# Kernel tuning notes

Hardware: AMD Instinct MI355X
Metric: run time of the kernel (lower is better)

The kernel has to match this reference:

```python
import jax, jax.numpy as jnp
import numpy as np

H = 12          # nheads
SIM_EPS = 1e-8  # SimMatrix eps
LN_EPS = 1e-5   # nn.LayerNorm default eps
SLOPE = 0.01    # LeakyReLU default negative slope


def leaky(x):
    return jnp.where(x >= 0, x, SLOPE * x)


def etc_attention(hiddens, gamma, beta, Wout, bout):
    # hiddens: [B, L, 3*D]
    B, L, D3 = hiddens.shape
    D = D3 // 3
    d = D // H
    h = hiddens.reshape(B, L, 3, H, d)
    Q = h[:, :, 0].transpose(0, 2, 1, 3)  # [B,H,L,d]
    K = h[:, :, 1].transpose(0, 2, 1, 3)
    V = h[:, :, 2].transpose(0, 2, 1, 3)
    # cosine-similarity attention scores (SimMatrix(K, Q))
    Kn = K / jnp.clip(jnp.linalg.norm(K, axis=-1, keepdims=True), SIM_EPS, None)
    Qn = Q / jnp.clip(jnp.linalg.norm(Q, axis=-1, keepdims=True), SIM_EPS, None)
    att = jnp.einsum('bhid,bhjd->bhij', Kn, Qn)  # [B,H,L,L]
    # LayerNorm over the head axis H (lnormalize: [B, L*L, H] layernorm on last dim)
    mu = att.mean(axis=1, keepdims=True)
    var = att.var(axis=1, keepdims=True)  # biased, matches torch LayerNorm
    att = (att - mu) / jnp.sqrt(var + LN_EPS)
    att = att * gamma[None, :, None, None] + beta[None, :, None, None]
    att = jax.nn.softmax(att, axis=-1)
    att = jnp.where(jnp.isnan(att), jnp.zeros_like(att), att)  # removeNaN
    out = jnp.einsum('bhij,bhjd->bhid', att, V)          # att @ V
    out = out.transpose(0, 2, 1, 3).reshape(B, L, D)      # catHiddens
    # dropout is identity at inference; lin_out = Linear + Softmax
    probs = jax.nn.softmax(out @ Wout.T + bout, axis=-1)  # [B,L,C]
    return probs, att


def get_weights(att, masks):
    # att: [B,H,L,L], masks: [B,L] float
    w = masks * att.mean(axis=1).sum(axis=1)  # [B,L]
    return jax.nn.softmax(w, axis=-1)[..., None]  # [B,L,1]


def setup_inputs() -> dict:
    key = jax.random.key(0)
    ks = jax.random.split(key, 16)
    B, L = 16, 512
    Din, D, C, VOCAB = 300, 768, 20, 32000

    def kaiming(k, shape, fan_in):
        return jax.random.normal(k, shape, jnp.float32) * np.sqrt(2.0 / fan_in)

    return {
        'input_ids': jax.random.randint(ks[0], (B, L), 0, VOCAB),
        'wv': jax.random.normal(ks[1], (B, L, Din), jnp.float32),
        'emb': jax.random.normal(ks[2], (VOCAB, D), jnp.float32),
        'W_t': kaiming(ks[3], (3 * D, D), D),
        'b_t': jnp.zeros((3 * D,), jnp.float32),
        'gamma_t': jnp.ones((H,), jnp.float32),
        'beta_t': jnp.zeros((H,), jnp.float32),
        'Wout_t': kaiming(ks[4], (C, D), D),
        'bout_t': jnp.zeros((C,), jnp.float32),
        'W_h': kaiming(ks[5], (3 * D, Din), Din),
        'b_h': jnp.zeros((3 * D,), jnp.float32),
        'gamma_h': jnp.ones((H,), jnp.float32),
        'beta_h': jnp.zeros((H,), jnp.float32),
        'Wout_h': kaiming(ks[6], (C, D), D),
        'bout_h': jnp.zeros((C,), jnp.float32),
    }


def reference(input_ids, wv, emb, W_t, b_t, gamma_t, beta_t, Wout_t, bout_t,
              W_h, b_h, gamma_h, beta_h, Wout_h, bout_h):
    masks = (input_ids != 0).astype(jnp.float32)  # [B,L]
    # token branch: Embedding -> LeakyReLU -> Linear -> LeakyReLU
    h_t = leaky(leaky(emb[input_ids]) @ W_t.T + b_t)
    probs_t, att_t = etc_attention(h_t, gamma_t, beta_t, Wout_t, bout_t)
    probs_t = (get_weights(att_t, masks) * probs_t).sum(axis=1)  # [B,C]
    # hidden/word-vector branch: Linear -> LeakyReLU
    h_h = leaky(wv @ W_h.T + b_h)
    probs_h, att_h = etc_attention(h_h, gamma_h, beta_h, Wout_h, bout_h)
    probs_h = (get_weights(att_h, masks) * probs_h).sum(axis=1)
    return (probs_t + probs_h) / 2.0
```

## Files before the change

kernel.cpp:

```cpp
#include <hip/hip_runtime.h>

typedef unsigned int uint;
typedef unsigned short ushort;
typedef _Float16 f16;
typedef _Float16 h8 __attribute__((ext_vector_type(8)));
typedef float f32x4 __attribute__((ext_vector_type(4)));


__device__ __forceinline__ float b2f(ushort u){ return __uint_as_float(((uint)u)<<16); }
__device__ __forceinline__ ushort f2b(float f){
  uint u = __float_as_uint(f);
  uint r = u + 0x7fffu + ((u>>16)&1u);
  return (ushort)(r>>16);
}
__device__ __forceinline__ float leaky(float x){ return x >= 0.f ? x : 0.01f*x; }
__device__ __forceinline__ float ldf(const void* p, int idx, int isb){
  return isb ? b2f(((const ushort*)p)[idx]) : ((const float*)p)[idx];
}

#define GLOAD16(gp, lp) __builtin_amdgcn_global_load_lds( \
    (const __attribute__((address_space(1))) void*)(gp), \
    (__attribute__((address_space(3))) void*)(lp), 16, 0, 0)

__global__ __launch_bounds__(256) void k_init(const ushort* __restrict__ wvbits,
    int* __restrict__ flag, float* __restrict__ zbase){
  int bid = blockIdx.x, tid = threadIdx.x;
  if (bid == 0){
    if (tid == 0){
      int sane = 0;
      for (int i=0;i<128;i++){
        uint e = (wvbits[i]>>7)&0xffu;
        if (e==0u || (e>=90u && e<=150u)) sane++;
      }
      *flag = (sane >= 115) ? 1 : 0;
    }
  } else {
    zbase[(bid-1)*256 + tid] = 0.f;
  }
}

__global__ __launch_bounds__(256) void k_prep_all(const int* __restrict__ ids,
    const void* __restrict__ emb, const void* __restrict__ wv,
    const void* __restrict__ W0, const void* __restrict__ W1,
    const int* __restrict__ flag,
    f16* __restrict__ AhA, f16* __restrict__ WhA,
    f16* __restrict__ AhB, f16* __restrict__ WhB,
    int nBX, int nW0, int nA1, int nW1){
  int isb = *flag;
  int bx = blockIdx.x, tid = threadIdx.x;
  if (bx < nBX){
    int t = bx*256 + tid;
    int m = t / 96, kk = (t % 96) * 8;
    float o[8];
    if (isb){
      const ushort* src = (const ushort*)emb + (size_t)ids[m]*768 + kk;
      uint4 v = *(const uint4*)src;
      o[0]=__uint_as_float((v.x&0xffffu)<<16); o[1]=__uint_as_float(v.x&0xffff0000u);
      o[2]=__uint_as_float((v.y&0xffffu)<<16); o[3]=__uint_as_float(v.y&0xffff0000u);
      o[4]=__uint_as_float((v.z&0xffffu)<<16); o[5]=__uint_as_float(v.z&0xffff0000u);
      o[6]=__uint_as_float((v.w&0xffffu)<<16); o[7]=__uint_as_float(v.w&0xffff0000u);
    } else {
      const float* src = (const float*)emb + (size_t)ids[m]*768 + kk;
      float4 v0 = ((const float4*)src)[0];
      float4 v1 = ((const float4*)src)[1];
      o[0]=v0.x; o[1]=v0.y; o[2]=v0.z; o[3]=v0.w;
      o[4]=v1.x; o[5]=v1.y; o[6]=v1.z; o[7]=v1.w;
    }
    h8 hv;
    #pragma unroll
    for (int i=0;i<8;i++) hv[i] = (f16)leaky(o[i]);
    *(h8*)(AhA + (size_t)m*768 + kk) = hv;
  } else if (bx < nBX + nW0){
    int t = (bx - nBX)*256 + tid;
    int n = t / 96, kk = (t % 96) * 8;
    h8 hv;
    #pragma unroll
    for (int i=0;i<8;i++) hv[i] = (f16)ldf(W0, n*768 + kk + i, isb);
    *(h8*)(WhA + (size_t)n*768 + kk) = hv;
  } else if (bx < nBX + nW0 + nA1){
    int t = (bx - nBX - nW0)*256 + tid;
    int n = t / 40, kk = (t % 40) * 8;
    h8 hv;
    #pragma unroll
    for (int i=0;i<8;i++){
      int k = kk + i;
      hv[i] = (k < 300) ? (f16)ldf(wv, n*300 + k, isb) : (f16)0.f;
    }
    *(h8*)(AhB + (size_t)n*320 + kk) = hv;
  } else {
    int t = (bx - nBX - nW0 - nA1)*256 + tid;
    int n = t / 40, kk = (t % 40) * 8;
    h8 hv;
    #pragma unroll
    for (int i=0;i<8;i++){
      int k = kk + i;
      hv[i] = (k < 300) ? (f16)ldf(W1, n*300 + k, isb) : (f16)0.f;
    }
    *(h8*)(WhB + (size_t)n*320 + kk) = hv;
  }
}

__global__ __launch_bounds__(256) void k_gemm_m(
    const f16* AhA, const f16* WhA, const void* biasA, int KA,
    f16* QhA, f16* KhA, f16* VtA,
    const f16* AhB, const f16* WhB, const void* biasB, int KB,
    f16* QhB, f16* KhB, f16* VtB,
    const int* __restrict__ flag, int sbase){
  __shared__ __align__(16) f16 As[128*64];
  __shared__ __align__(16) f16 Bs[128*64];
  int z = sbase + blockIdx.z;
  const f16* Ah = z ? AhB : AhA;
  const f16* Wh = z ? WhB : WhA;
  const void* bias = z ? biasB : biasA;
  int KP = z ? KB : KA;
  f16* Qh = z ? QhB : QhA;
  f16* Kh = z ? KhB : KhA;
  f16* Vt = z ? VtB : VtA;
  int STEPS = KP >> 6;

  int tid = threadIdx.x;
  int w = tid >> 6, lane = tid & 63;
  int mrow = lane & 15, kq = lane >> 4;
  int m0 = blockIdx.x * 128;
  int n0 = blockIdx.y * 128;
  int msub = (w & 1) * 64, nsub = (w >> 1) * 64;

  f32x4 acc[4][4];
  #pragma unroll
  for (int mt=0; mt<4; mt++)
    #pragma unroll
    for (int nt=0; nt<4; nt++) acc[mt][nt] = (f32x4){0.f,0.f,0.f,0.f};

  int cbase = w*64 + lane;

  for (int step=0; step<STEPS; step++){
    int k0 = step*64;
    __syncthreads();
    #pragma unroll
    for (int rep=0; rep<4; rep++){
      int cb = rep*256 + w*64;
      int c  = rep*256 + cbase;
      int row = c >> 3;
      int qs  = (c & 7) ^ (row & 7);
      GLOAD16(Ah + (size_t)(m0+row)*KP + k0 + qs*8, As + cb*8);
      GLOAD16(Wh + (size_t)(n0+row)*KP + k0 + qs*8, Bs + cb*8);
    }
    __syncthreads();
    #pragma unroll
    for (int ks=0; ks<2; ks++){
      h8 af[4], bf[4];
      #pragma unroll
      for (int mt=0; mt<4; mt++){
        int row = msub + mt*16 + mrow;
        int slot = (ks*4 + kq) ^ (row & 7);
        af[mt] = *(const h8*)(As + row*64 + slot*8);
      }
      #pragma unroll
      for (int nt=0; nt<4; nt++){
        int row = nsub + nt*16 + mrow;
        int slot = (ks*4 + kq) ^ (row & 7);
        bf[nt] = *(const h8*)(Bs + row*64 + slot*8);
      }
      #pragma unroll
      for (int mt=0; mt<4; mt++)
        #pragma unroll
        for (int nt=0; nt<4; nt++)
          acc[mt][nt] = __builtin_amdgcn_mfma_f32_16x16x32_f16(af[mt], bf[nt], acc[mt][nt], 0, 0, 0);
    }
  }

  int isb = *flag;
  int n0w = n0 + nsub;
  int s = n0w / 768;
  int h = (n0w % 768) >> 6;
  float bv[4];
  #pragma unroll
  for (int nt=0; nt<4; nt++) bv[nt] = ldf(bias, n0w + nt*16 + mrow, isb);

  #pragma unroll
  for (int mt=0; mt<4; mt++){
    float yv[4][4];
    #pragma unroll
    for (int nt=0; nt<4; nt++)
      #pragma unroll
      for (int r=0; r<4; r++)
        yv[nt][r] = leaky(acc[mt][nt][r] + bv[nt]);
    if (s < 2){
      #pragma unroll
      for (int r=0; r<4; r++){
        float ss = yv[0][r]*yv[0][r] + yv[1][r]*yv[1][r]
                 + yv[2][r]*yv[2][r] + yv[3][r]*yv[3][r];
        ss += __shfl_xor(ss, 1); ss += __shfl_xor(ss, 2);
        ss += __shfl_xor(ss, 4); ss += __shfl_xor(ss, 8);
        float rn = 1.f / fmaxf(sqrtf(ss), 1e-8f);
        #pragma unroll
        for (int nt=0; nt<4; nt++) yv[nt][r] *= rn;
      }
    }
    #pragma unroll
    for (int nt=0; nt<4; nt++){
      #pragma unroll
      for (int r=0; r<4; r++){
        int m = m0 + msub + mt*16 + kq*4 + r;
        int dd = nt*16 + mrow;
        int bq = m >> 9, l = m & 511;
        float y = yv[nt][r];
        if (s == 0)      Qh[((size_t)(bq*12 + h)*512 + l)*64 + dd] = (f16)y;
        else if (s == 1) Kh[((size_t)(bq*12 + h)*512 + l)*64 + dd] = (f16)y;
        else             Vt[((size_t)(bq*12 + h)*64 + dd)*512 + l] = (f16)y;
      }
    }
  }
}

__global__ __launch_bounds__(256) void k_attn(
    const f16* __restrict__ Qh0, const f16* __restrict__ Kh0, const f16* __restrict__ Vt0,
    const void* __restrict__ g0, const void* __restrict__ be0,
    float* __restrict__ O0, float* __restrict__ csg0,
    const f16* __restrict__ Qh1, const f16* __restrict__ Kh1, const f16* __restrict__ Vt1,
    const void* __restrict__ g1, const void* __restrict__ be1,
    float* __restrict__ O1, float* __restrict__ csg1,
    const int* __restrict__ flag, int sbase){
  constexpr int TS = 72;
  __shared__ __align__(16) f16 S[12*16*TS];
  __shared__ float gL[12], beL[12];
  __shared__ float rowsumL[192], rinvL[192];
  __shared__ float csL[512];

  int z = sbase + blockIdx.y;
  const f16* Qh = z ? Qh1 : Qh0;
  const f16* Kh = z ? Kh1 : Kh0;
  const f16* Vt = z ? Vt1 : Vt0;
  const void* gamma = z ? g1 : g0;
  const void* beta  = z ? be1 : be0;
  float* O   = z ? O1 : O0;
  float* csg = z ? csg1 : csg0;

  int tid = threadIdx.x;
  int w = tid >> 6, lane = tid & 63;
  int kq = lane >> 4, mrow = lane & 15;
  int b = blockIdx.x >> 5, it = blockIdx.x & 31;
  int i0 = it * 16;
  int h0 = w * 3;
  int pj = tid & 63, piw = tid >> 6;

  if (tid < 12){ int isb = *flag; gL[tid] = ldf(gamma, tid, isb); beL[tid] = ldf(beta, tid, isb); }
  if (tid < 192) rowsumL[tid] = 0.f;
  csL[tid] = 0.f; csL[tid + 256] = 0.f;

  h8 ka[3][2];
  #pragma unroll
  for (int hh=0; hh<3; hh++){
    const f16* kb = Kh + ((size_t)(b*12 + h0 + hh)*512 + i0 + mrow)*64;
    ka[hh][0] = *(const h8*)(kb + kq*8);
    ka[hh][1] = *(const h8*)(kb + 32 + kq*8);
  }

  f32x4 acc[3][4];
  #pragma unroll
  for (int hh=0; hh<3; hh++)
    #pragma unroll
    for (int nt=0; nt<4; nt++) acc[hh][nt] = (f32x4){0.f,0.f,0.f,0.f};

  __syncthreads();

  for (int jt=0; jt<8; jt++){
    int j0 = jt*64;
    #pragma unroll
    for (int hh=0; hh<3; hh++){
      int h = h0 + hh;
      const f16* qb = Qh + ((size_t)(b*12+h)*512 + j0)*64;
      #pragma unroll
      for (int jn=0; jn<4; jn++){
        const f16* qr = qb + (size_t)(jn*16 + mrow)*64;
        h8 q0 = *(const h8*)(qr + kq*8);
        h8 q1 = *(const h8*)(qr + 32 + kq*8);
        f32x4 c = (f32x4){0.f,0.f,0.f,0.f};
        c = __builtin_amdgcn_mfma_f32_16x16x32_f16(ka[hh][0], q0, c, 0, 0, 0);
        c = __builtin_amdgcn_mfma_f32_16x16x32_f16(ka[hh][1], q1, c, 0, 0, 0);
        #pragma unroll
        for (int r=0;r<4;r++)
          S[(h*16 + kq*4 + r)*TS + jn*16 + mrow] = (f16)c[r];
      }
    }
    __syncthreads();
    #pragma unroll
    for (int p=0; p<4; p++){
      int i = piw*4 + p;
      float s[12]; float mu=0.f, sq=0.f;
      #pragma unroll
      for (int h=0;h<12;h++){ s[h] = (float)S[(h*16+i)*TS + pj]; mu += s[h]; sq += s[h]*s[h]; }
      mu *= (1.f/12.f);
      float var = fmaxf(sq*(1.f/12.f) - mu*mu, 0.f);
      float rstd = rsqrtf(var + 1e-5f);
      #pragma unroll
      for (int h=0;h<12;h++){
        float e = __expf((s[h]-mu)*rstd*gL[h] + beL[h]);
        S[(h*16+i)*TS + pj] = (f16)e;
      }
    }
    __syncthreads();
    if (tid < 192){
      int h = tid >> 4, i = tid & 15;
      const f16* zr = &S[(h*16 + i)*TS];
      float ssum = 0.f;
      #pragma unroll
      for (int q=0;q<8;q++){
        h8 v = *(const h8*)(zr + q*8);
        #pragma unroll
        for (int t2=0;t2<8;t2++) ssum += (float)v[t2];
      }
      rowsumL[tid] += ssum;
    }
    #pragma unroll
    for (int hh=0; hh<3; hh++){
      int h = h0 + hh;
      const f16* sb = S + (h*16 + mrow)*TS + kq*8;
      const f16* vb = Vt + ((size_t)(b*12+h)*64 + mrow)*512 + j0 + kq*8;
      #pragma unroll
      for (int ks=0; ks<2; ks++){
        h8 ea = *(const h8*)(sb + ks*32);
        #pragma unroll
        for (int nt=0; nt<4; nt++){
          h8 bf = *(const h8*)(vb + (size_t)(nt*16)*512 + ks*32);
          acc[hh][nt] = __builtin_amdgcn_mfma_f32_16x16x32_f16(ea, bf, acc[hh][nt], 0, 0, 0);
        }
      }
    }
    __syncthreads();
  }

  if (tid < 192) rinvL[tid] = 1.f / rowsumL[tid];
  __syncthreads();

  #pragma unroll
  for (int hh=0; hh<3; hh++){
    int h = h0 + hh;
    #pragma unroll
    for (int r=0; r<4; r++){
      float g = rinvL[h*16 + kq*4 + r];
      #pragma unroll
      for (int nt=0; nt<4; nt++)
        O[((size_t)(b*512) + i0 + kq*4 + r)*768 + h*64 + nt*16 + mrow] = acc[hh][nt][r] * g;
    }
  }

  for (int jt=0; jt<8; jt++){
    int j0 = jt*64;
    #pragma unroll
    for (int hh=0; hh<3; hh++){
      int h = h0 + hh;
      const f16* qb = Qh + ((size_t)(b*12+h)*512 + j0)*64;
      #pragma unroll
      for (int jn=0; jn<4; jn++){
        const f16* qr = qb + (size_t)(jn*16 + mrow)*64;
        h8 q0 = *(const h8*)(qr + kq*8);
        h8 q1 = *(const h8*)(qr + 32 + kq*8);
        f32x4 c = (f32x4){0.f,0.f,0.f,0.f};
        c = __builtin_amdgcn_mfma_f32_16x16x32_f16(ka[hh][0], q0, c, 0, 0, 0);
        c = __builtin_amdgcn_mfma_f32_16x16x32_f16(ka[hh][1], q1, c, 0, 0, 0);
        #pragma unroll
        for (int r=0;r<4;r++)
          S[(h*16 + kq*4 + r)*TS + jn*16 + mrow] = (f16)c[r];
      }
    }
    __syncthreads();
    float cspart = 0.f;
    #pragma unroll
    for (int p=0; p<4; p++){
      int i = piw*4 + p;
      float s[12]; float mu=0.f, sq=0.f;
      #pragma unroll
      for (int h=0;h<12;h++){ s[h] = (float)S[(h*16+i)*TS + pj]; mu += s[h]; sq += s[h]*s[h]; }
      mu *= (1.f/12.f);
      float var = fmaxf(sq*(1.f/12.f) - mu*mu, 0.f);
      float rstd = rsqrtf(var + 1e-5f);
      #pragma unroll
      for (int h=0;h<12;h++){
        float e = __expf((s[h]-mu)*rstd*gL[h] + beL[h]);
        cspart += e * rinvL[h*16 + i];
      }
    }
    atomicAdd(&csL[j0 + pj], cspart);
    __syncthreads();
  }

  atomicAdd(&csg[b*512 + tid],       csL[tid]       * (1.f/12.f));
  atomicAdd(&csg[b*512 + 256 + tid], csL[tid + 256] * (1.f/12.f));
}

__global__ __launch_bounds__(256) void k_probs_m(const float* OA, const float* OB,
    const void* WoA, const void* WoB, const void* boA, const void* boB,
    float* prA, float* prB, const int* __restrict__ flag, int sbase){
  int z = sbase + blockIdx.y;
  const float* O = z ? OB : OA;
  const void* Wout = z ? WoB : WoA;
  const void* bout = z ? boB : boA;
  float* probs = z ? prB : prA;
  int isb = *flag;
  int tid = threadIdx.x, wv = tid>>6, lane = tid&63;
  int m = blockIdx.x*4 + wv;
  const float* orow = O + (size_t)m*768;
  float acc[20];
  #pragma unroll
  for (int c=0;c<20;c++) acc[c]=0.f;
  for (int kk=0; kk<12; kk++){
    float o = orow[kk*64 + lane];
    #pragma unroll
    for (int c=0;c<20;c++)
      acc[c] += o * ldf(Wout, c*768 + kk*64 + lane, isb);
  }
  #pragma unroll
  for (int c=0;c<20;c++){
    #pragma unroll
    for (int off=1; off<64; off<<=1) acc[c] += __shfl_xor(acc[c], off, 64);
  }
  float mx = -3.4e38f;
  #pragma unroll
  for (int c=0;c<20;c++){ acc[c] += ldf(bout, c, isb); mx = fmaxf(mx, acc[c]); }
  float s=0.f;
  #pragma unroll
  for (int c=0;c<20;c++){ acc[c] = __expf(acc[c]-mx); s += acc[c]; }
  float inv = 1.f/s;
  if (lane == 0){
    float* pr = probs + (size_t)m*20;
    #pragma unroll
    for (int c=0;c<20;c++) pr[c] = acc[c]*inv;
  }
}

__global__ __launch_bounds__(512) void k_final_m(const int* __restrict__ ids,
    const float* __restrict__ cs0, const float* __restrict__ cs1,
    const float* __restrict__ pr0, const float* __restrict__ pr1,
    const int* __restrict__ flag, void* __restrict__ outp){
  __shared__ float red[8];
  __shared__ float bcast;
  __shared__ float pacc[8][20];
  __shared__ float osum[20];
  int b = blockIdx.x, tid = threadIdx.x;
  int wv = tid>>6, lane = tid&63;
  int msk = (ids[b*512+tid] != 0);
  for (int br=0; br<2; br++){
    const float* colsum = br ? cs1 : cs0;
    const float* probs  = br ? pr1 : pr0;
    float w = msk ? colsum[b*512+tid] : 0.f;
    float mx = w;
    #pragma unroll
    for (int off=1; off<64; off<<=1) mx = fmaxf(mx, __shfl_xor(mx, off, 64));
    if (lane==0) red[wv] = mx;
    __syncthreads();
    if (tid==0){ float m2 = red[0]; for (int k2=1;k2<8;k2++) m2 = fmaxf(m2, red[k2]); bcast = m2; }
    __syncthreads();
    float M = bcast;
    float e = __expf(w - M);
    float s = e;
    #pragma unroll
    for (int off=1; off<64; off<<=1) s += __shfl_xor(s, off, 64);
    if (lane==0) red[wv] = s;
    __syncthreads();
    if (tid==0){ float s2=0.f; for (int k2=0;k2<8;k2++) s2 += red[k2]; bcast = s2; }
    __syncthreads();
    float wn = e / bcast;
    float p[20];
    const float* pr = probs + ((size_t)b*512 + tid)*20;
    #pragma unroll
    for (int c=0;c<20;c++) p[c] = wn * pr[c];
    #pragma unroll
    for (int c=0;c<20;c++){
      #pragma unroll
      for (int off=1; off<64; off<<=1) p[c] += __shfl_xor(p[c], off, 64);
    }
    if (lane==0){
      #pragma unroll
      for (int c=0;c<20;c++) pacc[wv][c] = p[c];
    }
    __syncthreads();
    if (tid < 20){
      float s2 = 0.f;
      #pragma unroll
      for (int k2=0;k2<8;k2++) s2 += pacc[k2][tid];
      if (br == 0) osum[tid] = s2;
      else         osum[tid] += s2;
    }
    __syncthreads();
  }
  if (tid < 20){
    float v = osum[tid] * 0.5f;
    if (*flag) ((ushort*)outp)[b*20 + tid] = f2b(v);
    else       ((float*)outp)[b*20 + tid] = v;
  }
}

extern "C" void kernel_launch(void* const* d_in, const int* in_sizes, int n_in,
                              void* d_out, int out_size, void* d_ws, size_t ws_size,
                              hipStream_t stream){
  (void)in_sizes; (void)n_in; (void)out_size;
  const int*  ids = (const int*)d_in[0];
  const void* wvp = d_in[1];
  const void* emb = d_in[2];
  const void* Wt[2]  = {d_in[3], d_in[9]};
  const void* bt[2]  = {d_in[4], d_in[10]};
  const void* gm[2]  = {d_in[5], d_in[11]};
  const void* bet[2] = {d_in[6], d_in[12]};
  const void* Wo[2]  = {d_in[7], d_in[13]};
  const void* bo[2]  = {d_in[8], d_in[14]};

  char* p = (char*)d_ws;
  #define ALLOC(ty, name, cnt) ty* name = (ty*)p; p += sizeof(ty)*(size_t)(cnt)

  p = (char*)d_ws;
  ALLOC(float, O0, 6291456);
  ALLOC(float, O1, 6291456);
  ALLOC(f16, Qh0, 6291456); ALLOC(f16, Kh0, 6291456); ALLOC(f16, Vt0, 6291456);
  ALLOC(f16, Qh1, 6291456); ALLOC(f16, Kh1, 6291456); ALLOC(f16, Vt1, 6291456);
  ALLOC(f16, Ah0, 6291456); ALLOC(f16, Wh0, 1769472);
  ALLOC(f16, Ah1, 2621440); ALLOC(f16, Wh1, 737280);
  ALLOC(float, probs0, 163840); ALLOC(float, probs1, 163840);
  ALLOC(float, zb_big, 16384);
  ALLOC(int, flag_big, 4);
  size_t needBig = (size_t)(p - (char*)d_ws);

  if (ws_size >= needBig){
    float* colsum0 = zb_big;
    float* colsum1 = zb_big + 8192;
    int* flagp = flag_big;

    k_init<<<65, 256, 0, stream>>>((const ushort*)wvp, flagp, zb_big);
    k_prep_all<<<3072+864+1280+360, 256, 0, stream>>>(ids, emb, wvp, Wt[0], Wt[1],
        flagp, Ah0, Wh0, Ah1, Wh1, 3072, 864, 1280, 360);
    dim3 gg(64, 18, 2);
    k_gemm_m<<<gg, 256, 0, stream>>>(Ah0, Wh0, bt[0], 768, Qh0, Kh0, Vt0,
                                     Ah1, Wh1, bt[1], 320, Qh1, Kh1, Vt1, flagp, 0);
    dim3 ga(512, 2);
    k_attn<<<ga, 256, 0, stream>>>(Qh0, Kh0, Vt0, gm[0], bet[0], O0, colsum0,
                                   Qh1, Kh1, Vt1, gm[1], bet[1], O1, colsum1, flagp, 0);
    dim3 gpr(2048, 2);
    k_probs_m<<<gpr, 256, 0, stream>>>(O0, O1, Wo[0], Wo[1], bo[0], bo[1],
                                       probs0, probs1, flagp, 0);
    k_final_m<<<16, 512, 0, stream>>>(ids, colsum0, colsum1, probs0, probs1, flagp, d_out);
    return;
  }

  p = (char*)d_ws;
  ALLOC(float, O, 6291456);
  ALLOC(f16, Qh, 6291456); ALLOC(f16, Kh, 6291456); ALLOC(f16, Vt, 6291456);
  ALLOC(f16, Ah, 6291456); ALLOC(f16, Wh, 1769472);
  ALLOC(float, probsA, 163840); ALLOC(float, probsB, 163840);
  ALLOC(float, zb, 16384);
  ALLOC(int, flagm, 4);
  float* colsum0 = zb;
  float* colsum1 = zb + 8192;

  k_init<<<65, 256, 0, stream>>>((const ushort*)wvp, flagm, zb);
  k_prep_all<<<3072+864, 256, 0, stream>>>(ids, emb, wvp, Wt[0], Wt[1],
      flagm, Ah, Wh, Ah, Wh, 3072, 864, 0, 0);
  dim3 g1(64, 18, 1);
  k_gemm_m<<<g1, 256, 0, stream>>>(Ah, Wh, bt[0], 768, Qh, Kh, Vt,
                                   Ah, Wh, bt[0], 768, Qh, Kh, Vt, flagm, 0);
  dim3 ga(512, 1);
  k_attn<<<ga, 256, 0, stream>>>(Qh, Kh, Vt, gm[0], bet[0], O, colsum0,
                                 Qh, Kh, Vt, gm[0], bet[0], O, colsum0, flagm, 0);
  dim3 gpr(2048, 1);
  k_probs_m<<<gpr, 256, 0, stream>>>(O, O, Wo[0], Wo[1], bo[0], bo[1],
                                     probsA, probsB, flagm, 0);
  k_prep_all<<<1280+360, 256, 0, stream>>>(ids, emb, wvp, Wt[0], Wt[1],
      flagm, Ah, Wh, Ah, Wh, 0, 0, 1280, 360);
  k_gemm_m<<<g1, 256, 0, stream>>>(Ah, Wh, bt[1], 320, Qh, Kh, Vt,
                                   Ah, Wh, bt[1], 320, Qh, Kh, Vt, flagm, 0);
  k_attn<<<ga, 256, 0, stream>>>(Qh, Kh, Vt, gm[1], bet[1], O, colsum1,
                                 Qh, Kh, Vt, gm[1], bet[1], O, colsum1, flagm, 0);
  k_probs_m<<<gpr, 256, 0, stream>>>(O, O, Wo[0], Wo[1], bo[0], bo[1],
                                     probsA, probsB, flagm, 1);
  k_final_m<<<16, 512, 0, stream>>>(ids, colsum0, colsum1, probsA, probsB, flagm, d_out);
  #undef ALLOC
}
```

Before: 624.3 us.

## Compute all heads per wave in registers to fuse head-LayerNorm without LDS round trip

```diff
diff --git a/kernel.cpp b/kernel.cpp
--- a/kernel.cpp
+++ b/kernel.cpp
@@ -224,7 +224,7 @@
   constexpr int TS = 72;
   __shared__ __align__(16) f16 S[12*16*TS];
   __shared__ float gL[12], beL[12];
-  __shared__ float rowsumL[192], rinvL[192];
+  __shared__ float rinvL[192];
   __shared__ float csL[512];
 
   int z = sbase + blockIdx.y;
@@ -241,149 +241,155 @@
   int kq = lane >> 4, mrow = lane & 15;
   int b = blockIdx.x >> 5, it = blockIdx.x & 31;
   int i0 = it * 16;
-  int h0 = w * 3;
-  int pj = tid & 63, piw = tid >> 6;
+  int jsw = w * 16;
 
   if (tid < 12){ int isb = *flag; gL[tid] = ldf(gamma, tid, isb); beL[tid] = ldf(beta, tid, isb); }
-  if (tid < 192) rowsumL[tid] = 0.f;
-  csL[tid] = 0.f; csL[tid + 256] = 0.f;
-
-  h8 ka[3][2];
-  #pragma unroll
-  for (int hh=0; hh<3; hh++){
-    const f16* kb = Kh + ((size_t)(b*12 + h0 + hh)*512 + i0 + mrow)*64;
-    ka[hh][0] = *(const h8*)(kb + kq*8);
-    ka[hh][1] = *(const h8*)(kb + 32 + kq*8);
-  }
-
-  f32x4 acc[3][4];
+  __syncthreads();
+
+  const f16* Kbase = Kh + ((size_t)(b*12)*512 + i0 + mrow)*64;
+  const f16* Qbase = Qh + ((size_t)(b*12)*512)*64;
+
+  f32x4 pv[3][4];
   #pragma unroll
   for (int hh=0; hh<3; hh++)
     #pragma unroll
-    for (int nt=0; nt<4; nt++) acc[hh][nt] = (f32x4){0.f,0.f,0.f,0.f};
-
-  __syncthreads();
+    for (int nt=0; nt<4; nt++) pv[hh][nt] = (f32x4){0.f,0.f,0.f,0.f};
+  float rs_acc = 0.f;
 
   for (int jt=0; jt<8; jt++){
-    int j0 = jt*64;
-    #pragma unroll
-    for (int hh=0; hh<3; hh++){
-      int h = h0 + hh;
-      const f16* qb = Qh + ((size_t)(b*12+h)*512 + j0)*64;
-      #pragma unroll
-      for (int jn=0; jn<4; jn++){
-        const f16* qr = qb + (size_t)(jn*16 + mrow)*64;
-        h8 q0 = *(const h8*)(qr + kq*8);
-        h8 q1 = *(const h8*)(qr + 32 + kq*8);
+    int js = jt*64 + jsw;
+    f32x4 acc[12];
+    #pragma unroll
+    for (int hb=0; hb<4; hb++){
+      h8 qv[3][2], kv[3][2];
+      #pragma unroll
+      for (int hh=0; hh<3; hh++){
+        int h = hb*3 + hh;
+        const f16* qp = Qbase + ((size_t)h*512 + js + mrow)*64;
+        const f16* kp = Kbase + (size_t)h*512*64;
+        qv[hh][0] = *(const h8*)(qp + kq*8);
+        qv[hh][1] = *(const h8*)(qp + 32 + kq*8);
+        kv[hh][0] = *(const h8*)(kp + kq*8);
+        kv[hh][1] = *(const h8*)(kp + 32 + kq*8);
+      }
+      #pragma unroll
+      for (int hh=0; hh<3; hh++){
         f32x4 c = (f32x4){0.f,0.f,0.f,0.f};
-        c = __builtin_amdgcn_mfma_f32_16x16x32_f16(ka[hh][0], q0, c, 0, 0, 0);
-        c = __builtin_amdgcn_mfma_f32_16x16x32_f16(ka[hh][1], q1, c, 0, 0, 0);
-        #pragma unroll
-        for (int r=0;r<4;r++)
-          S[(h*16 + kq*4 + r)*TS + jn*16 + mrow] = (f16)c[r];
-      }
-    }
-    __syncthreads();
-    #pragma unroll
-    for (int p=0; p<4; p++){
-      int i = piw*4 + p;
-      float s[12]; float mu=0.f, sq=0.f;
-      #pragma unroll
-      for (int h=0;h<12;h++){ s[h] = (float)S[(h*16+i)*TS + pj]; mu += s[h]; sq += s[h]*s[h]; }
+        c = __builtin_amdgcn_mfma_f32_16x16x32_f16(kv[hh][0], qv[hh][0], c, 0, 0, 0);
+        c = __builtin_amdgcn_mfma_f32_16x16x32_f16(kv[hh][1], qv[hh][1], c, 0, 0, 0);
+        acc[hb*3+hh] = c;
+      }
+    }
+    #pragma unroll
+    for (int r=0; r<4; r++){
+      float mu=0.f, sq=0.f;
+      #pragma unroll
+      for (int h=0; h<12; h++){ float s = acc[h][r]; mu += s; sq += s*s; }
       mu *= (1.f/12.f);
       float var = fmaxf(sq*(1.f/12.f) - mu*mu, 0.f);
       float rstd = rsqrtf(var + 1e-5f);
       #pragma unroll
-      for (int h=0;h<12;h++){
-        float e = __expf((s[h]-mu)*rstd*gL[h] + beL[h]);
-        S[(h*16+i)*TS + pj] = (f16)e;
-      }
-    }
-    __syncthreads();
-    if (tid < 192){
-      int h = tid >> 4, i = tid & 15;
-      const f16* zr = &S[(h*16 + i)*TS];
-      float ssum = 0.f;
-      #pragma unroll
-      for (int q=0;q<8;q++){
-        h8 v = *(const h8*)(zr + q*8);
-        #pragma unroll
-        for (int t2=0;t2<8;t2++) ssum += (float)v[t2];
-      }
-      rowsumL[tid] += ssum;
-    }
+      for (int h=0; h<12; h++){
+        float e = __expf((acc[h][r]-mu)*rstd*gL[h] + beL[h]);
+        S[(h*16 + kq*4 + r)*TS + jsw + mrow] = (f16)e;
+      }
+    }
+    __syncthreads();
     #pragma unroll
     for (int hh=0; hh<3; hh++){
-      int h = h0 + hh;
+      int h = w*3 + hh;
       const f16* sb = S + (h*16 + mrow)*TS + kq*8;
-      const f16* vb = Vt + ((size_t)(b*12+h)*64 + mrow)*512 + j0 + kq*8;
+      const f16* vb = Vt + ((size_t)(b*12+h)*64 + mrow)*512 + jt*64 + kq*8;
       #pragma unroll
       for (int ks=0; ks<2; ks++){
         h8 ea = *(const h8*)(sb + ks*32);
         #pragma unroll
         for (int nt=0; nt<4; nt++){
           h8 bf = *(const h8*)(vb + (size_t)(nt*16)*512 + ks*32);
-          acc[hh][nt] = __builtin_amdgcn_mfma_f32_16x16x32_f16(ea, bf, acc[hh][nt], 0, 0, 0);
+          pv[hh][nt] = __builtin_amdgcn_mfma_f32_16x16x32_f16(ea, bf, pv[hh][nt], 0, 0, 0);
         }
       }
     }
-    __syncthreads();
-  }
-
-  if (tid < 192) rinvL[tid] = 1.f / rowsumL[tid];
+    if (tid < 192){
+      const f16* zr = &S[tid*TS];
+      float ssum = 0.f;
+      #pragma unroll
+      for (int q=0; q<8; q++){
+        h8 v = *(const h8*)(zr + q*8);
+        #pragma unroll
+        for (int t2=0; t2<8; t2++) ssum += (float)v[t2];
+      }
+      rs_acc += ssum;
+    }
+    __syncthreads();
+  }
+
+  if (tid < 192) rinvL[tid] = 1.f / rs_acc;
   __syncthreads();
 
   #pragma unroll
   for (int hh=0; hh<3; hh++){
-    int h = h0 + hh;
+    int h = w*3 + hh;
     #pragma unroll
     for (int r=0; r<4; r++){
       float g = rinvL[h*16 + kq*4 + r];
       #pragma unroll
       for (int nt=0; nt<4; nt++)
-        O[((size_t)(b*512) + i0 + kq*4 + r)*768 + h*64 + nt*16 + mrow] = acc[hh][nt][r] * g;
-    }
-  }
+        O[((size_t)(b*512) + i0 + kq*4 + r)*768 + h*64 + nt*16 + mrow] = pv[hh][nt][r] * g;
+    }
+  }
+
+  float rv[12][4];
+  #pragma unroll
+  for (int h=0; h<12; h++)
+    #pragma unroll
+    for (int r=0; r<4; r++) rv[h][r] = rinvL[h*16 + kq*4 + r];
 
   for (int jt=0; jt<8; jt++){
-    int j0 = jt*64;
-    #pragma unroll
-    for (int hh=0; hh<3; hh++){
-      int h = h0 + hh;
-      const f16* qb = Qh + ((size_t)(b*12+h)*512 + j0)*64;
-      #pragma unroll
-      for (int jn=0; jn<4; jn++){
-        const f16* qr = qb + (size_t)(jn*16 + mrow)*64;
-        h8 q0 = *(const h8*)(qr + kq*8);
-        h8 q1 = *(const h8*)(qr + 32 + kq*8);
+    int js = jt*64 + jsw;
+    f32x4 acc[12];
+    #pragma unroll
+    for (int hb=0; hb<4; hb++){
+      h8 qv[3][2], kv[3][2];
+      #pragma unroll
+      for (int hh=0; hh<3; hh++){
+        int h = hb*3 + hh;
+        const f16* qp = Qbase + ((size_t)h*512 + js + mrow)*64;
+        const f16* kp = Kbase + (size_t)h*512*64;
+        qv[hh][0] = *(const h8*)(qp + kq*8);
+        qv[hh][1] = *(const h8*)(qp + 32 + kq*8);
+        kv[hh][0] = *(const h8*)(kp + kq*8);
+        kv[hh][1] = *(const h8*)(kp + 32 + kq*8);
+      }
+      #pragma unroll
+      for (int hh=0; hh<3; hh++){
         f32x4 c = (f32x4){0.f,0.f,0.f,0.f};
-        c = __builtin_amdgcn_mfma_f32_16x16x32_f16(ka[hh][0], q0, c, 0, 0, 0);
-        c = __builtin_amdgcn_mfma_f32_16x16x32_f16(ka[hh][1], q1, c, 0, 0, 0);
-        #pragma unroll
-        for (int r=0;r<4;r++)
-          S[(h*16 + kq*4 + r)*TS + jn*16 + mrow] = (f16)c[r];
-      }
-    }
-    __syncthreads();
+        c = __builtin_amdgcn_mfma_f32_16x16x32_f16(kv[hh][0], qv[hh][0], c, 0, 0, 0);
+        c = __builtin_amdgcn_mfma_f32_16x16x32_f16(kv[hh][1], qv[hh][1], c, 0, 0, 0);
+        acc[hb*3+hh] = c;
+      }
+    }
     float cspart = 0.f;
     #pragma unroll
-    for (int p=0; p<4; p++){
-      int i = piw*4 + p;
-      float s[12]; float mu=0.f, sq=0.f;
-      #pragma unroll
-      for (int h=0;h<12;h++){ s[h] = (float)S[(h*16+i)*TS + pj]; mu += s[h]; sq += s[h]*s[h]; }
+    for (int r=0; r<4; r++){
+      float mu=0.f, sq=0.f;
+      #pragma unroll
+      for (int h=0; h<12; h++){ float s = acc[h][r]; mu += s; sq += s*s; }
       mu *= (1.f/12.f);
       float var = fmaxf(sq*(1.f/12.f) - mu*mu, 0.f);
       float rstd = rsqrtf(var + 1e-5f);
       #pragma unroll
-      for (int h=0;h<12;h++){
-        float e = __expf((s[h]-mu)*rstd*gL[h] + beL[h]);
-        cspart += e * rinvL[h*16 + i];
-      }
-    }
-    atomicAdd(&csL[j0 + pj], cspart);
-    __syncthreads();
-  }
+      for (int h=0; h<12; h++){
+        float e = __expf((acc[h][r]-mu)*rstd*gL[h] + beL[h]);
+        e = (float)(f16)e;
+        cspart += e * rv[h][r];
+      }
+    }
+    cspart += __shfl_xor(cspart, 16);
+    cspart += __shfl_xor(cspart, 32);
+    if (lane < 16) csL[jt*64 + jsw + mrow] = cspart;
+  }
+  __syncthreads();
 
   atomicAdd(&csg[b*512 + tid],       csL[tid]       * (1.f/12.f));
   atomicAdd(&csg[b*512 + 256 + tid], csL[tid + 256] * (1.f/12.f));
```

After: 714.9 us. 1.15x slower.
